# Performance work log

Measured on AMD Instinct MI355X. Metric: run time of the kernel, lower is better.

The kernel has to match this reference:

```python
import jax, jax.numpy as jnp
import numpy as np

H = 768; I = 3072; NH = 12; HD = H // NH; L = 2; V = 32000
N = 2048; NSUB = 8; SUBLEN = 256; WIDTH = 512; EPS = 1e-6


def rmsnorm(x, w):
    x32 = x.astype(jnp.float32)
    n = x32 * jax.lax.rsqrt(jnp.mean(x32 * x32, axis=-1, keepdims=True) + EPS)
    return (n * w).astype(x.dtype)


def fixed_pos_embedding(ages, dim):
    # inv_freq: [dim//2]; torch.linspace(0, 2, steps=dim//2)
    inv_freq = 1.0 / (10000.0 ** jnp.linspace(0.0, 2.0, dim // 2))
    t = ages[:, None] * inv_freq[None, :]              # [N, dim//2]
    # stack((s, s), -1).reshape -> duplicate each entry pairwise (interleaved)
    sin = jnp.repeat(jnp.sin(t), 2, axis=-1)[:, None, :]  # [N, 1, dim]
    cos = jnp.repeat(jnp.cos(t), 2, axis=-1)[:, None, :]
    return sin, cos


def apply_rope(x, sin, cos):
    # x: [N, heads, hd]; sin/cos: [N, 1, hd]
    x1 = x[..., 0::2]
    x2 = x[..., 1::2]
    rot = jnp.stack((-x2, x1), axis=-1).reshape(x.shape)
    return x * cos + rot * sin


def build_mask(subject_lengths, n):
    # block-diagonal (per subject) + causal local window of WIDTH
    csum = jnp.cumsum(subject_lengths)
    idx = jnp.arange(n)
    seg = jnp.searchsorted(csum, idx, side='right')   # subject id per token
    i = idx[:, None]; j = idx[None, :]
    same = seg[:, None] == seg[None, :]
    return same & (j <= i) & ((i - j) < WIDTH)        # [N, N] bool


def encoder_layer(x, time_data, sin, cos, mask, norm_w, W_in, W_out):
    h = rmsnorm(x, norm_w)
    all_time = jnp.concatenate((time_data, time_data ** 2), axis=-1)  # [N, 4]
    h = h.at[:, -all_time.shape[1]:].set(all_time.astype(h.dtype))
    t = h @ W_in                                      # [N, 2I + 3H]
    ff = t[:, : 2 * I]
    qkv = t[:, 2 * I:].reshape(-1, 3, NH, HD)
    q = apply_rope(qkv[:, 0], sin, cos)
    k = apply_rope(qkv[:, 1], sin, cos)
    v = qkv[:, 2]
    scores = jnp.einsum('qhd,khd->hqk', q, k) / jnp.sqrt(jnp.float32(HD))
    scores = jnp.where(mask[None, :, :], scores, -jnp.inf)
    probs = jax.nn.softmax(scores, axis=-1)
    attn = jnp.einsum('hqk,khd->qhd', probs, v).reshape(-1, H)
    x1, x2 = jnp.split(ff, 2, axis=-1)
    ffo = jax.nn.silu(x1) * x2                        # swiglu
    return jnp.concatenate((attn, ffo), axis=-1) @ W_out


def setup_inputs() -> dict:
    key = jax.random.key(0)
    ks = jax.random.split(key, 6)
    tokens = jax.random.randint(ks[0], (N,), 0, V)
    ages = jnp.sort(jax.random.uniform(ks[1], (N,), dtype=jnp.float32) * 100.0)
    time_data = jax.random.normal(ks[2], (N, 2), dtype=jnp.float32)
    subject_lengths = jnp.full((NSUB,), SUBLEN, dtype=jnp.int32)
    embed_table = jax.random.normal(ks[3], (V, H), dtype=jnp.float32) * 0.02
    in_norm_w = jnp.ones((H,), jnp.float32)
    out_norm_w = jnp.ones((H,), jnp.float32)
    layer_norm_w = jnp.ones((L, H), jnp.float32)
    layer_Win = jax.random.normal(ks[4], (L, H, 2 * I + 3 * H), dtype=jnp.float32) / np.sqrt(H)
    layer_Wout = jax.random.normal(ks[5], (L, H + I, H), dtype=jnp.float32) / np.sqrt(H + I)
    return dict(tokens=tokens, ages=ages, time_data=time_data,
                subject_lengths=subject_lengths, embed_table=embed_table,
                in_norm_w=in_norm_w, out_norm_w=out_norm_w,
                layer_norm_w=layer_norm_w, layer_Win=layer_Win, layer_Wout=layer_Wout)


def reference(tokens, ages, time_data, subject_lengths, embed_table,
              in_norm_w, out_norm_w, layer_norm_w, layer_Win, layer_Wout):
    x = embed_table[tokens]                           # [N, H]
    x = rmsnorm(x, in_norm_w)
    sin, cos = fixed_pos_embedding(ages, HD)
    mask = build_mask(subject_lengths, x.shape[0])
    for l in range(L):
        x = x + encoder_layer(x, time_data, sin, cos, mask,
                              layer_norm_w[l], layer_Win[l], layer_Wout[l])
    return rmsnorm(x, out_norm_w)
```

## Files before the change

kernel.cpp:

```cpp
#include <hip/hip_runtime.h>
#include <math.h>

typedef unsigned short ushort_t;
typedef float f32x4 __attribute__((ext_vector_type(4)));
typedef __bf16 bf16x8 __attribute__((ext_vector_type(8)));

#define DEVFN __device__ __forceinline__

DEVFN ushort_t f2bf(float f) {
  unsigned int u = __float_as_uint(f);
  u += 0x7FFFu + ((u >> 16) & 1u);
  return (ushort_t)(u >> 16);
}
DEVFN float bf2f(ushort_t u) { return __uint_as_float((unsigned int)u << 16); }

DEVFN void gload(const ushort_t* src, char* dst) {
  __builtin_amdgcn_global_load_lds(
      (const __attribute__((address_space(1))) unsigned int*)src,
      (__attribute__((address_space(3))) unsigned int*)dst, 16, 0, 0);
}

#define N_TOK  2048
#define HDIM   768
#define TCOLS  8448
#define FFI    3072
#define NHEADS 12
#define HD     64
#define NSEG   8
#define SEGLEN 256
#define ABCOLS 3840
#define NPART  6
#define KCHUNK 768

__global__ __launch_bounds__(256) void transpose_all(
    const float* __restrict__ Win, const float* __restrict__ Wout,
    ushort_t* __restrict__ winT, ushort_t* __restrict__ woutT) {
  __shared__ ushort_t tile[32][66];
  int id = blockIdx.x;
  const float* in; ushort_t* out; int R, C, tr, tc;
  if (id < 6336) {
    const int z = id / 3168; id -= z * 3168;
    R = HDIM; C = TCOLS;
    tr = (id / 264) * 64; tc = (id % 264) * 32;
    in = Win + (size_t)z * R * C; out = winT + (size_t)z * R * C;
  } else {
    id -= 6336;
    const int z = id / 1440; id -= z * 1440;
    R = ABCOLS; C = HDIM;
    tr = (id / 24) * 64; tc = (id % 24) * 32;
    in = Wout + (size_t)z * R * C; out = woutT + (size_t)z * R * C;
  }
  const int tx = threadIdx.x, ty = threadIdx.y;
#pragma unroll
  for (int i = 0; i < 8; ++i) {
    const int r = ty + i * 8;
    tile[tx][r] = f2bf(in[(size_t)(tr + r) * C + tc + tx]);
  }
  __syncthreads();
#pragma unroll
  for (int i = 0; i < 4; ++i) {
    const int c = ty + i * 8;
    ushort2 pk; pk.x = tile[c][2 * tx]; pk.y = tile[c][2 * tx + 1];
    *(ushort2*)(out + (size_t)(tc + c) * R + tr + 2 * tx) = pk;
  }
}

__global__ __launch_bounds__(256) void rms_init(
    const float* __restrict__ embed, const int* __restrict__ tokens,
    const float* __restrict__ ages,
    const float* __restrict__ in_nw, const float* __restrict__ layer_nw,
    const float* __restrict__ time_data,
    float* __restrict__ x, ushort_t* __restrict__ hbuf, float2* __restrict__ sctab) {
  const int row = blockIdx.x;
  if (threadIdx.x < 32) {
    const int k = threadIdx.x;
    const float e = (2.0f * (float)k) / 31.0f;
    const float t = ages[row] * expf(-e * logf(10000.0f));
    float2 cs; cs.x = cosf(t); cs.y = sinf(t);
    sctab[row * HD + 2 * k] = cs;
    sctab[row * HD + 2 * k + 1] = cs;
  }
  const float* src = embed + (size_t)tokens[row] * HDIM;
  __shared__ float part[4];
  float v[3]; float ss = 0.f;
#pragma unroll
  for (int i = 0; i < 3; ++i) { v[i] = src[threadIdx.x + i * 256]; ss += v[i] * v[i]; }
#pragma unroll
  for (int off = 1; off < 64; off <<= 1) ss += __shfl_xor(ss, off);
  if ((threadIdx.x & 63) == 0) part[threadIdx.x >> 6] = ss;
  __syncthreads();
  const float rs = rsqrtf((part[0] + part[1] + part[2] + part[3]) * (1.0f / HDIM) + 1e-6f);
  float y[3]; float ss2 = 0.f;
#pragma unroll
  for (int i = 0; i < 3; ++i) {
    const int c = threadIdx.x + i * 256;
    y[i] = v[i] * rs * in_nw[c];
    x[(size_t)row * HDIM + c] = y[i];
    ss2 += y[i] * y[i];
  }
#pragma unroll
  for (int off = 1; off < 64; off <<= 1) ss2 += __shfl_xor(ss2, off);
  __syncthreads();
  if ((threadIdx.x & 63) == 0) part[threadIdx.x >> 6] = ss2;
  __syncthreads();
  const float rs2 = rsqrtf((part[0] + part[1] + part[2] + part[3]) * (1.0f / HDIM) + 1e-6f);
#pragma unroll
  for (int i = 0; i < 3; ++i) {
    const int c = threadIdx.x + i * 256;
    float val = y[i] * rs2 * layer_nw[c];
    if (c >= HDIM - 4) {
      const float td = time_data[row * 2 + (c & 1)];
      val = (c >= HDIM - 2) ? td * td : td;
    }
    hbuf[(size_t)row * HDIM + c] = f2bf(val);
  }
}

__global__ __launch_bounds__(256) void rms_fused(
    const ushort_t* __restrict__ cpartb, float* __restrict__ x,
    const float* __restrict__ w, const float* __restrict__ time_data,
    float* __restrict__ out_f32, ushort_t* __restrict__ out_bf16, const int mode) {
  const int row = blockIdx.x;
  const size_t stride = (size_t)N_TOK * HDIM;
  float v[3]; float ss = 0.f;
#pragma unroll
  for (int i = 0; i < 3; ++i) {
    const size_t idx = (size_t)row * HDIM + threadIdx.x + i * 256;
    float s = x[idx];
#pragma unroll
    for (int z = 0; z < NPART; ++z) s += bf2f(cpartb[z * stride + idx]);
    if (mode == 1) x[idx] = s;
    v[i] = s; ss += s * s;
  }
#pragma unroll
  for (int off = 1; off < 64; off <<= 1) ss += __shfl_xor(ss, off);
  __shared__ float part[4];
  if ((threadIdx.x & 63) == 0) part[threadIdx.x >> 6] = ss;
  __syncthreads();
  const float rs = rsqrtf((part[0] + part[1] + part[2] + part[3]) * (1.0f / HDIM) + 1e-6f);
#pragma unroll
  for (int i = 0; i < 3; ++i) {
    const int c = threadIdx.x + i * 256;
    float val = v[i] * rs * w[c];
    if (mode == 1) {
      if (c >= HDIM - 4) {
        const float td = time_data[row * 2 + (c & 1)];
        val = (c >= HDIM - 2) ? td * td : td;
      }
      out_bf16[(size_t)row * HDIM + c] = f2bf(val);
    } else {
      out_f32[(size_t)row * HDIM + c] = val;
    }
  }
}

#define G1_NT 24
#define G1_ABYT 8192
#define G1_BUF  20480

DEVFN int swz64(int p) {
  const int g = ((p >> 6) & 3) ^ ((p >> 8) & 3);
  return p ^ (g << 4);
}
DEVFN int ffmap(int vr) {
  return (vr < 2 * FFI) ? ((((vr >> 4) & 1) * FFI) + ((vr >> 5) << 4) + (vr & 15)) : vr;
}

DEVFN void g1f_stage(const ushort_t* __restrict__ A, const ushort_t* __restrict__ BT,
                     int m0, int n0, int kt_el, char* buf, int tid) {
#pragma unroll
  for (int i = 0; i < 2; ++i) {
    const int q = swz64(i * 4096 + tid * 16);
    gload(A + (size_t)(m0 + (q >> 6)) * HDIM + kt_el + ((q & 63) >> 1),
          buf + i * 4096 + ((tid >> 6) << 10));
  }
#pragma unroll
  for (int i = 0; i < 3; ++i) {
    const int q = swz64(i * 4096 + tid * 16);
    const int vr = n0 + (q >> 6);
    gload(BT + (size_t)ffmap(vr) * HDIM + kt_el + ((q & 63) >> 1),
          buf + G1_ABYT + i * 4096 + ((tid >> 6) << 10));
  }
}

__global__ __launch_bounds__(256, 3) void gemm1f(
    const ushort_t* __restrict__ A, const ushort_t* __restrict__ BT,
    const float2* __restrict__ sctab,
    ushort_t* __restrict__ ab, ushort_t* __restrict__ qr,
    ushort_t* __restrict__ kr, ushort_t* __restrict__ vT) {
  __shared__ __align__(16) char smem[2 * G1_BUF];
  const int tid = threadIdx.x;
  const int l = tid & 63, l15 = l & 15, l4 = l >> 4;
  const int wid = tid >> 6, wr = wid >> 1, wc = wid & 1;
  const int bid = (int)blockIdx.x;
  const int wg = (bid & 7) * 88 + (bid >> 3);
  const int nt = wg >> 4, mt = wg & 15;
  const int m0 = mt * 128, n0 = nt * 192;

  f32x4 acc[4][6] = {};

  g1f_stage(A, BT, m0, n0, 0,  smem, tid);
  g1f_stage(A, BT, m0, n0, 32, smem + G1_BUF, tid);
  asm volatile("s_waitcnt vmcnt(5)" ::: "memory");
  __builtin_amdgcn_s_barrier();
  __builtin_amdgcn_sched_barrier(0);

  for (int t = 0; t < G1_NT; ++t) {
    const char* bufA = smem + (t & 1) * G1_BUF;
    const char* bufB = bufA + G1_ABYT;
    bf16x8 a4[4], b6[6];
#pragma unroll
    for (int m = 0; m < 4; ++m) {
      const int p = (wr * 64 + m * 16 + l15) * 64 + l4 * 16;
      a4[m] = *(const bf16x8*)(bufA + swz64(p));
    }
#pragma unroll
    for (int n = 0; n < 6; ++n) {
      const int p = (wc * 96 + n * 16 + l15) * 64 + l4 * 16;
      b6[n] = *(const bf16x8*)(bufB + swz64(p));
    }
#pragma unroll
    for (int m = 0; m < 4; ++m)
#pragma unroll
      for (int n = 0; n < 6; ++n)
        acc[m][n] = __builtin_amdgcn_mfma_f32_16x16x32_bf16(a4[m], b6[n], acc[m][n], 0, 0, 0);

    if (t == G1_NT - 1) break;
    __builtin_amdgcn_sched_barrier(0);
    __builtin_amdgcn_s_barrier();
    if (t + 2 < G1_NT) {
      g1f_stage(A, BT, m0, n0, (t + 2) * 32, smem + (t & 1) * G1_BUF, tid);
      asm volatile("s_waitcnt vmcnt(5)" ::: "memory");
    } else {
      asm volatile("s_waitcnt vmcnt(0)" ::: "memory");
    }
    __builtin_amdgcn_s_barrier();
    __builtin_amdgcn_sched_barrier(0);
  }

  if (nt < 32) {
#pragma unroll
    for (int m = 0; m < 4; ++m)
#pragma unroll
      for (int np = 0; np < 3; ++np) {
        const int colj = (nt * 6 + wc * 3 + np) * 16 + l15;
#pragma unroll
        for (int r = 0; r < 4; ++r) {
          const float x1 = acc[m][2 * np][r], x2 = acc[m][2 * np + 1][r];
          const float sv = x1 / (1.f + __expf(-x1)) * x2;
          const int row = m0 + wr * 64 + m * 16 + l4 * 4 + r;
          ab[(size_t)row * ABCOLS + HDIM + colj] = f2bf(sv);
        }
      }
  } else {
#pragma unroll
    for (int n = 0; n < 6; ++n) {
      const int gcol = (nt - 32) * 192 + wc * 96 + n * 16;
      const int g = gcol >> 6;
      const int typ = g / NHEADS, h = g - typ * NHEADS;
      const int d = (gcol & 63) + l15;
      if (typ == 2) {
#pragma unroll
        for (int m = 0; m < 4; ++m) {
          ushort4 pk;
          pk.x = f2bf(acc[m][n][0]); pk.y = f2bf(acc[m][n][1]);
          pk.z = f2bf(acc[m][n][2]); pk.w = f2bf(acc[m][n][3]);
          const int row0 = m0 + wr * 64 + m * 16 + l4 * 4;
          *(ushort4*)(vT + ((size_t)h * HD + d) * N_TOK + row0) = pk;
        }
      } else {
        ushort_t* dst = (typ == 0) ? qr : kr;
        const float sgn = (l15 & 1) ? 1.f : -1.f;
#pragma unroll
        for (int m = 0; m < 4; ++m)
#pragma unroll
          for (int r = 0; r < 4; ++r) {
            const float val = acc[m][n][r];
            const float partner = __shfl_xor(val, 1);
            const int row = m0 + wr * 64 + m * 16 + l4 * 4 + r;
            const float2 cs = sctab[row * HD + d];
            dst[((size_t)h * N_TOK + row) * HD + d] = f2bf(val * cs.x + sgn * partner * cs.y);
          }
      }
    }
  }
}

#define G2_BUF 32768

DEVFN int swz128(int p) { return p ^ (((p >> 7) & 7) << 4); }

DEVFN void g2_stage(const ushort_t* __restrict__ A, const ushort_t* __restrict__ BT,
                    int m0, int n0, int kt_el, char* buf, int tid) {
#pragma unroll
  for (int i = 0; i < 8; ++i) {
    const int p = i * 4096 + tid * 16;
    const bool isA = p < 16384;
    const int q = swz128(isA ? p : p - 16384);
    const int row = q >> 7, colel = (q & 127) >> 1;
    const ushort_t* src = (isA ? A + (size_t)(m0 + row) * ABCOLS
                               : BT + (size_t)(n0 + row) * ABCOLS) + kt_el + colel;
    gload(src, buf + i * 4096 + ((tid >> 6) << 10));
  }
}

DEVFN void g2_body(const ushort_t* __restrict__ A, const ushort_t* __restrict__ BT,
                   char* smem, int m0, int n0, int kt0, int NT,
                   ushort_t* __restrict__ outp, int tid) {
  const int l = tid & 63, l15 = l & 15, l4 = l >> 4;
  const int w = tid >> 6, wr = w >> 1, wc = w & 1;
  f32x4 acc[4][4] = {};

  g2_stage(A, BT, m0, n0, kt0, smem, tid);
  g2_stage(A, BT, m0, n0, kt0 + 64, smem + G2_BUF, tid);
  asm volatile("s_waitcnt vmcnt(8)" ::: "memory");
  __builtin_amdgcn_s_barrier();
  __builtin_amdgcn_sched_barrier(0);

  for (int t = 0; t < NT; ++t) {
    const char* bufA = smem + (t & 1) * G2_BUF;
    const char* bufB = bufA + 16384;
    bf16x8 af[4][2], bv[4][2];
#pragma unroll
    for (int kk = 0; kk < 2; ++kk) {
#pragma unroll
      for (int mi = 0; mi < 4; ++mi) {
        const int p = (wr * 64 + mi * 16 + l15) * 128 + kk * 64 + l4 * 16;
        af[mi][kk] = *(const bf16x8*)(bufA + swz128(p));
      }
#pragma unroll
      for (int ni = 0; ni < 4; ++ni) {
        const int p = (wc * 64 + ni * 16 + l15) * 128 + kk * 64 + l4 * 16;
        bv[ni][kk] = *(const bf16x8*)(bufB + swz128(p));
      }
    }
#pragma unroll
    for (int kk = 0; kk < 2; ++kk)
#pragma unroll
      for (int mi = 0; mi < 4; ++mi)
#pragma unroll
        for (int ni = 0; ni < 4; ++ni)
          acc[mi][ni] = __builtin_amdgcn_mfma_f32_16x16x32_bf16(af[mi][kk], bv[ni][kk], acc[mi][ni], 0, 0, 0);

    if (t == NT - 1) break;
    __builtin_amdgcn_sched_barrier(0);
    __builtin_amdgcn_s_barrier();
    if (t + 2 < NT) {
      g2_stage(A, BT, m0, n0, kt0 + (t + 2) * 64, smem + (t & 1) * G2_BUF, tid);
      asm volatile("s_waitcnt vmcnt(8)" ::: "memory");
    } else {
      asm volatile("s_waitcnt vmcnt(0)" ::: "memory");
    }
    __builtin_amdgcn_s_barrier();
    __builtin_amdgcn_sched_barrier(0);
  }

#pragma unroll
  for (int mi = 0; mi < 4; ++mi)
#pragma unroll
    for (int ni = 0; ni < 4; ++ni)
#pragma unroll
      for (int r = 0; r < 4; ++r) {
        const int row = m0 + wr * 64 + mi * 16 + l4 * 4 + r;
        const int col = n0 + wc * 64 + ni * 16 + l15;
        outp[(size_t)row * HDIM + col] = f2bf(acc[mi][ni][r]);
      }
}

DEVFN void attn_one(const ushort_t* __restrict__ qr, const ushort_t* __restrict__ kr,
                    const ushort_t* __restrict__ vT, ushort_t* __restrict__ ab,
                    int h, int seg, int qt, ushort_t* Pw, int l15, int l4) {
  const int qrow0 = seg * SEGLEN + qt * 16;
  bf16x8 aq[2];
#pragma unroll
  for (int kk = 0; kk < 2; ++kk)
    aq[kk] = *(const bf16x8*)(qr + ((size_t)h * N_TOK + qrow0 + l15) * HD + kk * 32 + l4 * 8);

  f32x4 o[4] = {};
  float m_run[4], l_run[4];
#pragma unroll
  for (int r = 0; r < 4; ++r) { m_run[r] = -1e30f; l_run[r] = 0.f; }

  const int kbmax = qt >> 2;
  for (int kb = 0; kb <= kbmax; ++kb) {
    bf16x8 bk[4][2];
#pragma unroll
    for (int ni = 0; ni < 4; ++ni)
#pragma unroll
      for (int kk = 0; kk < 2; ++kk)
        bk[ni][kk] = *(const bf16x8*)(kr + ((size_t)h * N_TOK + seg * SEGLEN + kb * 64 + ni * 16 + l15) * HD + kk * 32 + l4 * 8);
    f32x4 s[4] = {};
#pragma unroll
    for (int ni = 0; ni < 4; ++ni)
#pragma unroll
      for (int kk = 0; kk < 2; ++kk)
        s[ni] = __builtin_amdgcn_mfma_f32_16x16x32_bf16(aq[kk], bk[ni][kk], s[ni], 0, 0, 0);

    const bool diag = (kb == kbmax);
#pragma unroll
    for (int ni = 0; ni < 4; ++ni)
#pragma unroll
      for (int r = 0; r < 4; ++r) {
        float v = s[ni][r] * 0.125f;
        if (diag) {
          const int qrow = qt * 16 + l4 * 4 + r;
          const int jcol = kb * 64 + ni * 16 + l15;
          if (jcol > qrow) v = -1e30f;
        }
        s[ni][r] = v;
      }

    float sc_[4];
#pragma unroll
    for (int r = 0; r < 4; ++r) {
      float pm = fmaxf(fmaxf(s[0][r], s[1][r]), fmaxf(s[2][r], s[3][r]));
      pm = fmaxf(pm, __shfl_xor(pm, 1));
      pm = fmaxf(pm, __shfl_xor(pm, 2));
      pm = fmaxf(pm, __shfl_xor(pm, 4));
      pm = fmaxf(pm, __shfl_xor(pm, 8));
      const float mn = fmaxf(m_run[r], pm);
      sc_[r] = __expf(m_run[r] - mn);
      m_run[r] = mn;
    }
#pragma unroll
    for (int ni = 0; ni < 4; ++ni)
#pragma unroll
      for (int r = 0; r < 4; ++r)
        s[ni][r] = __expf(s[ni][r] - m_run[r]);
#pragma unroll
    for (int r = 0; r < 4; ++r) {
      float ls = s[0][r] + s[1][r] + s[2][r] + s[3][r];
      ls += __shfl_xor(ls, 1);
      ls += __shfl_xor(ls, 2);
      ls += __shfl_xor(ls, 4);
      ls += __shfl_xor(ls, 8);
      l_run[r] = l_run[r] * sc_[r] + ls;
    }
#pragma unroll
    for (int ni = 0; ni < 4; ++ni)
#pragma unroll
      for (int r = 0; r < 4; ++r)
        o[ni][r] *= sc_[r];

#pragma unroll
    for (int ni = 0; ni < 4; ++ni)
#pragma unroll
      for (int r = 0; r < 4; ++r)
        Pw[(l4 * 4 + r) * 64 + ni * 16 + l15] = f2bf(s[ni][r]);

    bf16x8 pa[2], bv[4][2];
#pragma unroll
    for (int k2 = 0; k2 < 2; ++k2)
      pa[k2] = *(const bf16x8*)(&Pw[l15 * 64 + k2 * 32 + l4 * 8]);
#pragma unroll
    for (int ni = 0; ni < 4; ++ni)
#pragma unroll
      for (int k2 = 0; k2 < 2; ++k2)
        bv[ni][k2] = *(const bf16x8*)(vT + ((size_t)h * HD + ni * 16 + l15) * N_TOK + seg * SEGLEN + kb * 64 + k2 * 32 + l4 * 8);
#pragma unroll
    for (int ni = 0; ni < 4; ++ni)
#pragma unroll
      for (int k2 = 0; k2 < 2; ++k2)
        o[ni] = __builtin_amdgcn_mfma_f32_16x16x32_bf16(pa[k2], bv[ni][k2], o[ni], 0, 0, 0);
  }

#pragma unroll
  for (int ni = 0; ni < 4; ++ni)
#pragma unroll
    for (int r = 0; r < 4; ++r) {
      const int row = qrow0 + l4 * 4 + r;
      const int col = h * HD + ni * 16 + l15;
      ab[(size_t)row * ABCOLS + col] = f2bf(o[ni][r] / l_run[r]);
    }
}

__global__ __launch_bounds__(256) void fused_mid(
    const ushort_t* __restrict__ ab, const ushort_t* __restrict__ woutT,
    ushort_t* __restrict__ cpartb,
    const ushort_t* __restrict__ qr, const ushort_t* __restrict__ kr,
    const ushort_t* __restrict__ vT, ushort_t* __restrict__ ab_out) {
  __shared__ __align__(16) char smem[2 * G2_BUF];
  const int b = (int)blockIdx.x;
  const int tid = threadIdx.x;
  if (b < 192) {
    const int h = b % NHEADS;
    const int r2 = b / NHEADS;
    const int seg = r2 & 7, p = r2 >> 3;
    const int w = tid >> 6, l = tid & 63;
    const int l15 = l & 15, l4 = l >> 4;
    ushort_t* Pw = (ushort_t*)smem + w * (16 * 64);
    attn_one(qr, kr, vT, ab_out, h, seg, p * 4 + w, Pw, l15, l4);
    attn_one(qr, kr, vT, ab_out, h, seg, (3 - p) * 4 + w, Pw, l15, l4);
  } else {
    const int idx = b - 192;
    const int z = 1 + (idx / 96);
    const int rem = idx % 96;
    const int n0 = (rem % 6) * 128, m0 = (rem / 6) * 128;
    g2_body(ab, woutT, smem, m0, n0, z * KCHUNK, 12,
            cpartb + (size_t)(z - 1) * N_TOK * HDIM, tid);
  }
}

__global__ __launch_bounds__(256) void gemm2_z0(
    const ushort_t* __restrict__ ab, const ushort_t* __restrict__ woutT,
    ushort_t* __restrict__ cpartb) {
  __shared__ __align__(16) char smem[2 * G2_BUF];
  const int b = (int)blockIdx.x;
  const int half = b / 96, rem = b % 96;
  const int n0 = (rem % 6) * 128, m0 = (rem / 6) * 128;
  g2_body(ab, woutT, smem, m0, n0, half * 384, 6,
          cpartb + (size_t)(4 + half) * N_TOK * HDIM, threadIdx.x);
}

extern "C" void kernel_launch(void* const* d_in, const int* in_sizes, int n_in,
                              void* d_out, int out_size, void* d_ws, size_t ws_size,
                              hipStream_t stream) {
  const int*   tokens   = (const int*)d_in[0];
  const float* ages     = (const float*)d_in[1];
  const float* time_d   = (const float*)d_in[2];
  const float* embed    = (const float*)d_in[4];
  const float* in_nw    = (const float*)d_in[5];
  const float* out_nw   = (const float*)d_in[6];
  const float* layer_nw = (const float*)d_in[7];
  const float* Win      = (const float*)d_in[8];
  const float* Wout     = (const float*)d_in[9];
  float* out = (float*)d_out;

  char* ws = (char*)d_ws;
  float*    x      = (float*)   (ws + 0);
  ushort_t* hbuf   = (ushort_t*)(ws + 6291456);
  float2*   sctab  = (float2*)  (ws + 9437184);
  ushort_t* cpartb = (ushort_t*)(ws + 10485760);
  ushort_t* ab     = (ushort_t*)(ws + 29360128);
  ushort_t* qrb    = (ushort_t*)(ws + 45088768);
  ushort_t* krb    = (ushort_t*)(ws + 48234496);
  ushort_t* vTb    = (ushort_t*)(ws + 51380224);
  ushort_t* winT   = (ushort_t*)(ws + 54525952);
  ushort_t* woutT  = (ushort_t*)(ws + 80478208);

  transpose_all<<<dim3(9216), dim3(32, 8), 0, stream>>>(Win, Wout, winT, woutT);
  rms_init<<<dim3(N_TOK), dim3(256), 0, stream>>>(embed, tokens, ages, in_nw, layer_nw,
                                                  time_d, x, hbuf, sctab);

  for (int lyr = 0; lyr < 2; ++lyr) {
    gemm1f<<<dim3(704), dim3(256), 0, stream>>>(hbuf, winT + (size_t)lyr * TCOLS * HDIM,
                                                sctab, ab, qrb, krb, vTb);
    fused_mid<<<dim3(576), dim3(256), 0, stream>>>(ab, woutT + (size_t)lyr * HDIM * ABCOLS,
                                                   cpartb, qrb, krb, vTb, ab);
    gemm2_z0<<<dim3(192), dim3(256), 0, stream>>>(ab, woutT + (size_t)lyr * HDIM * ABCOLS,
                                                  cpartb);
    if (lyr == 0)
      rms_fused<<<dim3(N_TOK), dim3(256), 0, stream>>>(cpartb, x, layer_nw + HDIM, time_d,
                                                       nullptr, hbuf, 1);
    else
      rms_fused<<<dim3(N_TOK), dim3(256), 0, stream>>>(cpartb, x, out_nw, nullptr,
                                                       out, nullptr, 2);
  }
}
```

Baseline: 186.5 us.

## Widen GEMM2 tiles, interleave attention blocks, merge preamble kernels, vectorize RMS

The output-projection GEMM tile grows from 128x128 to 128x192, so each wave computes 4x6 MFMA fragments with per-kk fragment loads. This cuts the GEMM2 block count and reuses A data across more columns, at the cost of more LDS and accumulator registers. Attention and GEMM2 blocks in the fused kernel are interleaved in a 3:4 pattern to balance work across CUs, and launch bounds now request two blocks per CU. The weight transpose and initial RMS norm are merged into one launch, and the RMS kernels switch to float4/ushort4 vector accesses with only 192 active threads.

```diff
diff --git a/kernel.cpp b/kernel.cpp
--- a/kernel.cpp
+++ b/kernel.cpp
@@ -32,87 +32,94 @@
 #define NPART  6
 #define KCHUNK 768
 
-__global__ __launch_bounds__(256) void transpose_all(
+__global__ __launch_bounds__(256) void preamble(
     const float* __restrict__ Win, const float* __restrict__ Wout,
-    ushort_t* __restrict__ winT, ushort_t* __restrict__ woutT) {
-  __shared__ ushort_t tile[32][66];
-  int id = blockIdx.x;
-  const float* in; ushort_t* out; int R, C, tr, tc;
-  if (id < 6336) {
-    const int z = id / 3168; id -= z * 3168;
-    R = HDIM; C = TCOLS;
-    tr = (id / 264) * 64; tc = (id % 264) * 32;
-    in = Win + (size_t)z * R * C; out = winT + (size_t)z * R * C;
-  } else {
-    id -= 6336;
-    const int z = id / 1440; id -= z * 1440;
-    R = ABCOLS; C = HDIM;
-    tr = (id / 24) * 64; tc = (id % 24) * 32;
-    in = Wout + (size_t)z * R * C; out = woutT + (size_t)z * R * C;
-  }
-  const int tx = threadIdx.x, ty = threadIdx.y;
-#pragma unroll
-  for (int i = 0; i < 8; ++i) {
-    const int r = ty + i * 8;
-    tile[tx][r] = f2bf(in[(size_t)(tr + r) * C + tc + tx]);
-  }
-  __syncthreads();
-#pragma unroll
-  for (int i = 0; i < 4; ++i) {
-    const int c = ty + i * 8;
-    ushort2 pk; pk.x = tile[c][2 * tx]; pk.y = tile[c][2 * tx + 1];
-    *(ushort2*)(out + (size_t)(tc + c) * R + tr + 2 * tx) = pk;
-  }
-}
-
-__global__ __launch_bounds__(256) void rms_init(
+    ushort_t* __restrict__ winT, ushort_t* __restrict__ woutT,
     const float* __restrict__ embed, const int* __restrict__ tokens,
     const float* __restrict__ ages,
     const float* __restrict__ in_nw, const float* __restrict__ layer_nw,
     const float* __restrict__ time_data,
     float* __restrict__ x, ushort_t* __restrict__ hbuf, float2* __restrict__ sctab) {
-  const int row = blockIdx.x;
-  if (threadIdx.x < 32) {
-    const int k = threadIdx.x;
+  const int tid = threadIdx.x;
+  if (blockIdx.x < 9216) {
+    __shared__ ushort_t tile[32][66];
+    int id = blockIdx.x;
+    const float* in; ushort_t* out; int R, C, tr, tc;
+    if (id < 6336) {
+      const int z = id / 3168; id -= z * 3168;
+      R = HDIM; C = TCOLS;
+      tr = (id / 264) * 64; tc = (id % 264) * 32;
+      in = Win + (size_t)z * R * C; out = winT + (size_t)z * R * C;
+    } else {
+      id -= 6336;
+      const int z = id / 1440; id -= z * 1440;
+      R = ABCOLS; C = HDIM;
+      tr = (id / 24) * 64; tc = (id % 24) * 32;
+      in = Wout + (size_t)z * R * C; out = woutT + (size_t)z * R * C;
+    }
+    const int tx = tid & 31, ty = tid >> 5;
+#pragma unroll
+    for (int i = 0; i < 8; ++i) {
+      const int r = ty + i * 8;
+      tile[tx][r] = f2bf(in[(size_t)(tr + r) * C + tc + tx]);
+    }
+    __syncthreads();
+#pragma unroll
+    for (int i = 0; i < 4; ++i) {
+      const int c = ty + i * 8;
+      ushort2 pk; pk.x = tile[c][2 * tx]; pk.y = tile[c][2 * tx + 1];
+      *(ushort2*)(out + (size_t)(tc + c) * R + tr + 2 * tx) = pk;
+    }
+    return;
+  }
+  const int row = blockIdx.x - 9216;
+  if (tid < 32) {
+    const int k = tid;
     const float e = (2.0f * (float)k) / 31.0f;
     const float t = ages[row] * expf(-e * logf(10000.0f));
     float2 cs; cs.x = cosf(t); cs.y = sinf(t);
     sctab[row * HD + 2 * k] = cs;
     sctab[row * HD + 2 * k + 1] = cs;
   }
+  __shared__ float part[4];
   const float* src = embed + (size_t)tokens[row] * HDIM;
-  __shared__ float part[4];
-  float v[3]; float ss = 0.f;
-#pragma unroll
-  for (int i = 0; i < 3; ++i) { v[i] = src[threadIdx.x + i * 256]; ss += v[i] * v[i]; }
+  float4 v = {0.f, 0.f, 0.f, 0.f};
+  const int c0 = tid * 4;
+  if (tid < 192) v = *(const float4*)(src + c0);
+  float ss = v.x * v.x + v.y * v.y + v.z * v.z + v.w * v.w;
 #pragma unroll
   for (int off = 1; off < 64; off <<= 1) ss += __shfl_xor(ss, off);
-  if ((threadIdx.x & 63) == 0) part[threadIdx.x >> 6] = ss;
+  if ((tid & 63) == 0) part[tid >> 6] = ss;
   __syncthreads();
   const float rs = rsqrtf((part[0] + part[1] + part[2] + part[3]) * (1.0f / HDIM) + 1e-6f);
-  float y[3]; float ss2 = 0.f;
-#pragma unroll
-  for (int i = 0; i < 3; ++i) {
-    const int c = threadIdx.x + i * 256;
-    y[i] = v[i] * rs * in_nw[c];
-    x[(size_t)row * HDIM + c] = y[i];
-    ss2 += y[i] * y[i];
-  }
+  float4 y = {0.f, 0.f, 0.f, 0.f};
+  if (tid < 192) {
+    y.x = v.x * rs * in_nw[c0]; y.y = v.y * rs * in_nw[c0 + 1];
+    y.z = v.z * rs * in_nw[c0 + 2]; y.w = v.w * rs * in_nw[c0 + 3];
+    *(float4*)(x + (size_t)row * HDIM + c0) = y;
+  }
+  float ss2 = y.x * y.x + y.y * y.y + y.z * y.z + y.w * y.w;
 #pragma unroll
   for (int off = 1; off < 64; off <<= 1) ss2 += __shfl_xor(ss2, off);
   __syncthreads();
-  if ((threadIdx.x & 63) == 0) part[threadIdx.x >> 6] = ss2;
+  if ((tid & 63) == 0) part[tid >> 6] = ss2;
   __syncthreads();
   const float rs2 = rsqrtf((part[0] + part[1] + part[2] + part[3]) * (1.0f / HDIM) + 1e-6f);
-#pragma unroll
-  for (int i = 0; i < 3; ++i) {
-    const int c = threadIdx.x + i * 256;
-    float val = y[i] * rs2 * layer_nw[c];
-    if (c >= HDIM - 4) {
-      const float td = time_data[row * 2 + (c & 1)];
-      val = (c >= HDIM - 2) ? td * td : td;
-    }
-    hbuf[(size_t)row * HDIM + c] = f2bf(val);
+  if (tid < 192) {
+    float val[4];
+#pragma unroll
+    for (int j = 0; j < 4; ++j) {
+      const int c = c0 + j;
+      float vv = ((const float*)&y)[j] * rs2 * layer_nw[c];
+      if (c >= HDIM - 4) {
+        const float td = time_data[row * 2 + (c & 1)];
+        vv = (c >= HDIM - 2) ? td * td : td;
+      }
+      val[j] = vv;
+    }
+    ushort4 pk;
+    pk.x = f2bf(val[0]); pk.y = f2bf(val[1]); pk.z = f2bf(val[2]); pk.w = f2bf(val[3]);
+    *(ushort4*)(hbuf + (size_t)row * HDIM + c0) = pk;
   }
 }
 
@@ -122,34 +129,44 @@
     float* __restrict__ out_f32, ushort_t* __restrict__ out_bf16, const int mode) {
   const int row = blockIdx.x;
   const size_t stride = (size_t)N_TOK * HDIM;
-  float v[3]; float ss = 0.f;
-#pragma unroll
-  for (int i = 0; i < 3; ++i) {
-    const size_t idx = (size_t)row * HDIM + threadIdx.x + i * 256;
-    float s = x[idx];
-#pragma unroll
-    for (int z = 0; z < NPART; ++z) s += bf2f(cpartb[z * stride + idx]);
-    if (mode == 1) x[idx] = s;
-    v[i] = s; ss += s * s;
-  }
+  const int tid = threadIdx.x;
+  const int c0 = tid * 4;
+  float4 s = {0.f, 0.f, 0.f, 0.f};
+  if (tid < 192) {
+    s = *(const float4*)(x + (size_t)row * HDIM + c0);
+#pragma unroll
+    for (int z = 0; z < NPART; ++z) {
+      const ushort4 p = *(const ushort4*)(cpartb + z * stride + (size_t)row * HDIM + c0);
+      s.x += bf2f(p.x); s.y += bf2f(p.y); s.z += bf2f(p.z); s.w += bf2f(p.w);
+    }
+    if (mode == 1) *(float4*)(x + (size_t)row * HDIM + c0) = s;
+  }
+  float ss = s.x * s.x + s.y * s.y + s.z * s.z + s.w * s.w;
 #pragma unroll
   for (int off = 1; off < 64; off <<= 1) ss += __shfl_xor(ss, off);
   __shared__ float part[4];
-  if ((threadIdx.x & 63) == 0) part[threadIdx.x >> 6] = ss;
+  if ((tid & 63) == 0) part[tid >> 6] = ss;
   __syncthreads();
   const float rs = rsqrtf((part[0] + part[1] + part[2] + part[3]) * (1.0f / HDIM) + 1e-6f);
-#pragma unroll
-  for (int i = 0; i < 3; ++i) {
-    const int c = threadIdx.x + i * 256;
-    float val = v[i] * rs * w[c];
+  if (tid < 192) {
+    float val[4];
+#pragma unroll
+    for (int j = 0; j < 4; ++j) {
+      const int c = c0 + j;
+      float vv = ((const float*)&s)[j] * rs * w[c];
+      if (mode == 1 && c >= HDIM - 4) {
+        const float td = time_data[row * 2 + (c & 1)];
+        vv = (c >= HDIM - 2) ? td * td : td;
+      }
+      val[j] = vv;
+    }
     if (mode == 1) {
-      if (c >= HDIM - 4) {
-        const float td = time_data[row * 2 + (c & 1)];
-        val = (c >= HDIM - 2) ? td * td : td;
-      }
-      out_bf16[(size_t)row * HDIM + c] = f2bf(val);
+      ushort4 pk;
+      pk.x = f2bf(val[0]); pk.y = f2bf(val[1]); pk.z = f2bf(val[2]); pk.w = f2bf(val[3]);
+      *(ushort4*)(out_bf16 + (size_t)row * HDIM + c0) = pk;
     } else {
-      out_f32[(size_t)row * HDIM + c] = val;
+      float4 o; o.x = val[0]; o.y = val[1]; o.z = val[2]; o.w = val[3];
+      *(float4*)(out_f32 + (size_t)row * HDIM + c0) = o;
     }
   }
 }
@@ -286,14 +303,14 @@
   }
 }
 
-#define G2_BUF 32768
+#define G2_BUF 40960
 
 DEVFN int swz128(int p) { return p ^ (((p >> 7) & 7) << 4); }
 
 DEVFN void g2_stage(const ushort_t* __restrict__ A, const ushort_t* __restrict__ BT,
                     int m0, int n0, int kt_el, char* buf, int tid) {
 #pragma unroll
-  for (int i = 0; i < 8; ++i) {
+  for (int i = 0; i < 10; ++i) {
     const int p = i * 4096 + tid * 16;
     const bool isA = p < 16384;
     const int q = swz128(isA ? p : p - 16384);
@@ -309,45 +326,43 @@
                    ushort_t* __restrict__ outp, int tid) {
   const int l = tid & 63, l15 = l & 15, l4 = l >> 4;
   const int w = tid >> 6, wr = w >> 1, wc = w & 1;
-  f32x4 acc[4][4] = {};
+  f32x4 acc[4][6] = {};
 
   g2_stage(A, BT, m0, n0, kt0, smem, tid);
   g2_stage(A, BT, m0, n0, kt0 + 64, smem + G2_BUF, tid);
-  asm volatile("s_waitcnt vmcnt(8)" ::: "memory");
+  asm volatile("s_waitcnt vmcnt(10)" ::: "memory");
   __builtin_amdgcn_s_barrier();
   __builtin_amdgcn_sched_barrier(0);
 
   for (int t = 0; t < NT; ++t) {
     const char* bufA = smem + (t & 1) * G2_BUF;
     const char* bufB = bufA + 16384;
-    bf16x8 af[4][2], bv[4][2];
 #pragma unroll
     for (int kk = 0; kk < 2; ++kk) {
+      bf16x8 af[4], bv[6];
 #pragma unroll
       for (int mi = 0; mi < 4; ++mi) {
         const int p = (wr * 64 + mi * 16 + l15) * 128 + kk * 64 + l4 * 16;
-        af[mi][kk] = *(const bf16x8*)(bufA + swz128(p));
-      }
-#pragma unroll
-      for (int ni = 0; ni < 4; ++ni) {
-        const int p = (wc * 64 + ni * 16 + l15) * 128 + kk * 64 + l4 * 16;
-        bv[ni][kk] = *(const bf16x8*)(bufB + swz128(p));
-      }
-    }
-#pragma unroll
-    for (int kk = 0; kk < 2; ++kk)
+        af[mi] = *(const bf16x8*)(bufA + swz128(p));
+      }
+#pragma unroll
+      for (int ni = 0; ni < 6; ++ni) {
+        const int p = (wc * 96 + ni * 16 + l15) * 128 + kk * 64 + l4 * 16;
+        bv[ni] = *(const bf16x8*)(bufB + swz128(p));
+      }
 #pragma unroll
       for (int mi = 0; mi < 4; ++mi)
 #pragma unroll
-        for (int ni = 0; ni < 4; ++ni)
-          acc[mi][ni] = __builtin_amdgcn_mfma_f32_16x16x32_bf16(af[mi][kk], bv[ni][kk], acc[mi][ni], 0, 0, 0);
+        for (int ni = 0; ni < 6; ++ni)
+          acc[mi][ni] = __builtin_amdgcn_mfma_f32_16x16x32_bf16(af[mi], bv[ni], acc[mi][ni], 0, 0, 0);
+    }
 
     if (t == NT - 1) break;
     __builtin_amdgcn_sched_barrier(0);
     __builtin_amdgcn_s_barrier();
     if (t + 2 < NT) {
       g2_stage(A, BT, m0, n0, kt0 + (t + 2) * 64, smem + (t & 1) * G2_BUF, tid);
-      asm volatile("s_waitcnt vmcnt(8)" ::: "memory");
+      asm volatile("s_waitcnt vmcnt(10)" ::: "memory");
     } else {
       asm volatile("s_waitcnt vmcnt(0)" ::: "memory");
     }
@@ -358,11 +373,11 @@
 #pragma unroll
   for (int mi = 0; mi < 4; ++mi)
 #pragma unroll
-    for (int ni = 0; ni < 4; ++ni)
+    for (int ni = 0; ni < 6; ++ni)
 #pragma unroll
       for (int r = 0; r < 4; ++r) {
         const int row = m0 + wr * 64 + mi * 16 + l4 * 4 + r;
-        const int col = n0 + wc * 64 + ni * 16 + l15;
+        const int col = n0 + wc * 96 + ni * 16 + l15;
         outp[(size_t)row * HDIM + col] = f2bf(acc[mi][ni][r]);
       }
 }
@@ -474,7 +489,7 @@
     }
 }
 
-__global__ __launch_bounds__(256) void fused_mid(
+__global__ __launch_bounds__(256, 2) void fused_mid(
     const ushort_t* __restrict__ ab, const ushort_t* __restrict__ woutT,
     ushort_t* __restrict__ cpartb,
     const ushort_t* __restrict__ qr, const ushort_t* __restrict__ kr,
@@ -482,9 +497,11 @@
   __shared__ __align__(16) char smem[2 * G2_BUF];
   const int b = (int)blockIdx.x;
   const int tid = threadIdx.x;
-  if (b < 192) {
-    const int h = b % NHEADS;
-    const int r2 = b / NHEADS;
+  const int sel = b % 7;
+  if (sel < 3) {
+    const int a = (b / 7) * 3 + sel;
+    const int h = a % NHEADS;
+    const int r2 = a / NHEADS;
     const int seg = r2 & 7, p = r2 >> 3;
     const int w = tid >> 6, l = tid & 63;
     const int l15 = l & 15, l4 = l >> 4;
@@ -492,22 +509,22 @@
     attn_one(qr, kr, vT, ab_out, h, seg, p * 4 + w, Pw, l15, l4);
     attn_one(qr, kr, vT, ab_out, h, seg, (3 - p) * 4 + w, Pw, l15, l4);
   } else {
-    const int idx = b - 192;
-    const int z = 1 + (idx / 96);
-    const int rem = idx % 96;
-    const int n0 = (rem % 6) * 128, m0 = (rem / 6) * 128;
+    const int f = (b / 7) * 4 + (sel - 3);
+    const int z = 1 + (f >> 6);
+    const int rem = f & 63;
+    const int n0 = (rem & 3) * 192, m0 = (rem >> 2) * 128;
     g2_body(ab, woutT, smem, m0, n0, z * KCHUNK, 12,
             cpartb + (size_t)(z - 1) * N_TOK * HDIM, tid);
   }
 }
 
-__global__ __launch_bounds__(256) void gemm2_z0(
+__global__ __launch_bounds__(256, 2) void gemm2_z0(
     const ushort_t* __restrict__ ab, const ushort_t* __restrict__ woutT,
     ushort_t* __restrict__ cpartb) {
   __shared__ __align__(16) char smem[2 * G2_BUF];
   const int b = (int)blockIdx.x;
-  const int half = b / 96, rem = b % 96;
-  const int n0 = (rem % 6) * 128, m0 = (rem / 6) * 128;
+  const int half = b >> 6, rem = b & 63;
+  const int n0 = (rem & 3) * 192, m0 = (rem >> 2) * 128;
   g2_body(ab, woutT, smem, m0, n0, half * 384, 6,
           cpartb + (size_t)(4 + half) * N_TOK * HDIM, threadIdx.x);
 }
@@ -538,16 +555,16 @@
   ushort_t* winT   = (ushort_t*)(ws + 54525952);
   ushort_t* woutT  = (ushort_t*)(ws + 80478208);
 
-  transpose_all<<<dim3(9216), dim3(32, 8), 0, stream>>>(Win, Wout, winT, woutT);
-  rms_init<<<dim3(N_TOK), dim3(256), 0, stream>>>(embed, tokens, ages, in_nw, layer_nw,
+  preamble<<<dim3(11264), dim3(256), 0, stream>>>(Win, Wout, winT, woutT,
+                                                  embed, tokens, ages, in_nw, layer_nw,
                                                   time_d, x, hbuf, sctab);
 
   for (int lyr = 0; lyr < 2; ++lyr) {
     gemm1f<<<dim3(704), dim3(256), 0, stream>>>(hbuf, winT + (size_t)lyr * TCOLS * HDIM,
                                                 sctab, ab, qrb, krb, vTb);
-    fused_mid<<<dim3(576), dim3(256), 0, stream>>>(ab, woutT + (size_t)lyr * HDIM * ABCOLS,
+    fused_mid<<<dim3(448), dim3(256), 0, stream>>>(ab, woutT + (size_t)lyr * HDIM * ABCOLS,
                                                    cpartb, qrb, krb, vTb, ab);
-    gemm2_z0<<<dim3(192), dim3(256), 0, stream>>>(ab, woutT + (size_t)lyr * HDIM * ABCOLS,
+    gemm2_z0<<<dim3(128), dim3(256), 0, stream>>>(ab, woutT + (size_t)lyr * HDIM * ABCOLS,
                                                   cpartb);
     if (lyr == 0)
       rms_fused<<<dim3(N_TOK), dim3(256), 0, stream>>>(cpartb, x, layer_nw + HDIM, time_d,
```

Measured after the change: 184.1 us. Within noise of the previous version (-1.3%).
